# Optimization experiments

Hardware: AMD Instinct MI355X
Metric: run time of the kernel (lower is better)

The kernel has to match this reference:

```python
import jax, jax.numpy as jnp
import numpy as np

# --- fixed model configuration (from init_kwargs) ---
NX, NY, NU, NP = 8, 8, 2, 5
DELTA = 0.01
PHO, CP, AR, AB = 5.0, 6.0, 3.0, 3.0
KR, KB, TD, QR, QB = 2.5, 1.5, 300.0, 200.0, 200.0
CAF, TF = 6.0, 320.0
YMEAN = jnp.array([50.0, 1.0, 0.5, 313.0, 50.0, 1.0, 0.5, 313.0], jnp.float32)
YSTD = jnp.array([2.0, 0.2, 0.1, 4.0, 2.0, 0.2, 0.1, 4.0], jnp.float32)
UMEAN = jnp.array([10.0, 5.0], jnp.float32)
USTD = jnp.array([1.0, 0.5], jnp.float32)


def _fg(x, u):
    """Grey-box CSTR+flash ODE RHS. x: [B,8] scaled, u: [B,2] scaled."""
    x = x * YSTD + YMEAN
    u = u * USTD + UMEAN
    Hr, CAr, CBr, Tr = x[..., 0:1], x[..., 1:2], x[..., 2:3], x[..., 3:4]
    Hb, CAb, CBb, Tb = x[..., 4:5], x[..., 5:6], x[..., 6:7], x[..., 7:8]
    F, D = u[..., 0:1], u[..., 1:2]
    Fr = KR * jnp.sqrt(Hr)
    Fb = KB * jnp.sqrt(Hb)
    dHr = (F + D - Fr) / AR
    dCAr = (F * (CAF - CAr) - D * CAr) / (AR * Hr)
    dCBr = (-F * CBr - D * CBr) / (AR * Hr)
    dTr = (F * (TF - Tr) + D * (TD - Tr)) / (AR * Hr) + QR / (PHO * AR * CP * Hr)
    dHb = (Fr - Fb - D) / AB
    dCAb = (Fr * (CAr - CAb) + D * CAb) / (AB * Hb)
    dCBb = (Fr * (CBr - CBb) + D * CBb) / (AB * Hb)
    dTb = Fr * (Tr - Tb) / (AB * Hb) + QB / (PHO * AB * CP * Hb)
    xdot = jnp.concatenate([dHr, dCAr, dCBr, dTr, dHb, dCAb, dCBb, dTb], axis=-1)
    return xdot / YSTD


def setup_inputs() -> dict:
    key = jax.random.key(0)
    ks = jax.random.split(key, 6)
    B, T = 2048, 128
    d_in, d_h = NX + NP * (NY + NU) + NU, 128  # 60, 128
    useq = jax.random.normal(ks[0], (B, T, NU), jnp.float32)
    xGz0 = jax.random.normal(ks[1], (B, NX + NP * (NY + NU)), jnp.float32)
    W1 = jax.random.normal(ks[2], (d_in, d_h), jnp.float32) * (1.0 / np.sqrt(d_in))
    b1 = jnp.zeros((d_h,), jnp.float32)
    W2 = jax.random.normal(ks[3], (d_h, d_h), jnp.float32) * (1.0 / np.sqrt(d_h))
    b2 = jnp.zeros((d_h,), jnp.float32)
    W3 = jax.random.normal(ks[4], (d_h, NX), jnp.float32) * (1.0 / np.sqrt(d_h))
    b3 = jnp.zeros((NX,), jnp.float32)
    return {"useq": useq, "xGz0": xGz0, "W1": W1, "b1": b1,
            "W2": W2, "b2": b2, "W3": W3, "b3": b3}


def reference(useq, xGz0, W1, b1, W2, b2, W3, b3):
    def fnn(inp):
        h = jnp.tanh(inp @ W1 + b1)
        h = jnp.tanh(h @ W2 + b2)
        return h @ W3 + b3

    def interp(yfull):  # [B,(Np+1)*Ny] -> [B,Np*Ny]
        B = yfull.shape[0]
        y = yfull.reshape(B, NP + 1, NY)
        return (0.5 * (y[:, :-1] + y[:, 1:])).reshape(B, NP * NY)

    def step(xGz, u):
        xG = xGz[:, :NX]
        z = xGz[:, NX:]
        ypseq = z[:, :NP * NY]
        upseq = z[:, NP * NY:]
        # k1
        k1 = _fg(xG, u) + fnn(jnp.concatenate((xG, z, u), axis=-1))
        # interpolated half-step past sequence
        yp_interp = interp(jnp.concatenate((ypseq, xG), axis=-1))
        z_half = jnp.concatenate((yp_interp, upseq), axis=-1)
        x2 = xG + DELTA * (k1 / 2)
        k2 = _fg(x2, u) + fnn(jnp.concatenate((x2, z_half, u), axis=-1))
        x3 = xG + DELTA * (k2 / 2)
        k3 = _fg(x3, u) + fnn(jnp.concatenate((x3, z_half, u), axis=-1))
        yp_shift = jnp.concatenate((ypseq[:, NY:], xG), axis=-1)
        z_full = jnp.concatenate((yp_shift, upseq), axis=-1)
        x4 = xG + DELTA * k3
        k4 = _fg(x4, u) + fnn(jnp.concatenate((x4, z_full, u), axis=-1))
        y = xG
        xGplus = xG + (DELTA / 6) * (k1 + 2 * k2 + 2 * k3 + k4)
        zplus = jnp.concatenate((yp_shift, upseq[:, NU:], u), axis=-1)
        return jnp.concatenate((xGplus, zplus), axis=-1), y

    u_t = jnp.swapaxes(useq, 0, 1)  # [T,B,Nu]
    _, ys = jax.lax.scan(step, xGz0, u_t)  # ys: [T,B,Ny]
    return jnp.swapaxes(ys, 0, 1)  # [B,T,Ny]
```

## Files before the change

### kernel.cpp

```cpp
#include <hip/hip_runtime.h>
#include <math.h>

#define BLOCK 256
#define ROWS 16

typedef __attribute__((ext_vector_type(8))) short s16x8;
typedef __attribute__((ext_vector_type(4))) float f32x4;

static constexpr int O_W1  = 0;
static constexpr int O_W2  = 4608;
static constexpr int O_W3  = 13312;
static constexpr int O_INB = 14400;
static constexpr int O_H1  = 14976;
static constexpr int O_H2  = 16064;
static constexpr int O_B1  = 17152;
static constexpr int O_B2  = 17280;
static constexpr int O_B3  = 17408;
static constexpr int O_SU  = 17416;
static constexpr int O_YPM = 21512;
static constexpr int O_UPM = 22152;
static constexpr int O_XM  = 22344;
static constexpr int O_NNP = 22472;
static constexpr int LDSN  = 22984;

__device__ __forceinline__ unsigned short f2bf(float f) {
  unsigned u = __float_as_uint(f);
  return (unsigned short)((u + 0x7fffu + ((u >> 16) & 1u)) >> 16);
}
__device__ __forceinline__ unsigned cvt_pk_bf16(float lo, float hi) {
  unsigned r;
  asm("v_cvt_pk_bf16_f32 %0, %1, %2" : "=v"(r) : "v"(lo), "v"(hi));
  return r;
}
__device__ __forceinline__ float tanh_fast(float x) {
  float e = __builtin_amdgcn_exp2f(x * 2.88539008177792681f);
  return fmaf(-2.f, __builtin_amdgcn_rcpf(e + 1.f), 1.f);
}

#define MFMA16(A, B, C) __builtin_amdgcn_mfma_f32_16x16x32_bf16((A), (B), (C), 0, 0, 0)

#define PACK_OUT(C, BV, DST) {                        \
  float t0_ = tanh_fast((C)[0] + (BV).x);             \
  float t1_ = tanh_fast((C)[1] + (BV).y);             \
  float t2_ = tanh_fast((C)[2] + (BV).z);             \
  float t3_ = tanh_fast((C)[3] + (BV).w);             \
  uint2 pk_; pk_.x = cvt_pk_bf16(t0_, t1_);           \
  pk_.y = cvt_pk_bf16(t2_, t3_);                      \
  *(uint2*)(DST) = pk_; }

extern "C" __global__ void __launch_bounds__(BLOCK, 1)
cstr_rk4_mfma4(const float* __restrict__ useq, const float* __restrict__ xGz0,
               const float* __restrict__ W1, const float* __restrict__ b1,
               const float* __restrict__ W2, const float* __restrict__ b2,
               const float* __restrict__ W3, const float* __restrict__ b3,
               float* __restrict__ out)
{
  extern __shared__ float smf[];
  unsigned* smu = (unsigned*)smf;
  unsigned short* smh = (unsigned short*)smf;

  unsigned short* w1h = smh + 2 * O_W1;
  unsigned short* w2h = smh + 2 * O_W2;
  unsigned short* w3h = smh + 2 * O_W3;
  unsigned short* inh = smh + 2 * O_INB;
  unsigned short* h1h = smh + 2 * O_H1;
  unsigned short* h2h = smh + 2 * O_H2;
  unsigned* h1u = smu + O_H1;
  unsigned* h2u = smu + O_H2;
  float* b1s = smf + O_B1;
  float* b2s = smf + O_B2;
  float* b3s = smf + O_B3;
  float* su  = smf + O_SU;
  float* ypm = smf + O_YPM;
  float* upm = smf + O_UPM;
  float* xm  = smf + O_XM;
  float* nnp = smf + O_NNP;

  const int tid  = threadIdx.x;
  const int w    = tid >> 6;
  const int l    = tid & 63;
  const int nn   = l & 15;
  const int hh   = l >> 4;
  const int base = blockIdx.x * ROWS;

  for (int i = tid; i < 128 * 72; i += BLOCK) {
    int j = i / 72, k = i % 72;
    w1h[i] = (k < 60) ? f2bf(W1[k * 128 + j]) : (unsigned short)0;
  }
  for (int i = tid; i < 128 * 136; i += BLOCK) {
    int j = i / 136, k = i % 136;
    w2h[i] = (k < 128) ? f2bf(W2[k * 128 + j]) : (unsigned short)0;
  }
  for (int i = tid; i < 16 * 136; i += BLOCK) {
    int o = i / 136, k = i % 136;
    w3h[i] = (o < 8 && k < 128) ? f2bf(W3[k * 8 + o]) : (unsigned short)0;
  }
  if (tid < 128) { b1s[tid] = b1[tid]; b2s[tid] = b2[tid]; }
  if (tid < 8) b3s[tid] = b3[tid];
  for (int i = tid; i < ROWS * 256; i += BLOCK) su[i] = useq[(size_t)base * 256 + i];
  for (int i = tid; i < ROWS * 40; i += BLOCK) {
    int r_ = i / 40, ci = i % 40;
    ypm[i] = xGz0[(size_t)(base + r_) * 58 + 8 + ci];
  }
  for (int i = tid; i < ROWS * 12; i += BLOCK) {
    int r_ = i / 12, ci = i % 12;
    upm[i] = (ci < 10) ? xGz0[(size_t)(base + r_) * 58 + 48 + ci] : 0.f;
  }
  for (int i = tid; i < ROWS * 8; i += BLOCK)
    xm[i] = xGz0[(size_t)(base + (i >> 3)) * 58 + (i & 7)];
  for (int i = tid; i < 16 * 72; i += BLOCK) {
    int n_ = i / 72, k = i % 72;
    unsigned short v = 0;
    if (k < 58)      v = f2bf(xGz0[(size_t)(base + n_) * 58 + k]);
    else if (k < 60) v = f2bf(useq[(size_t)(base + n_) * 256 + (k - 58)]);
    inh[i] = v;
  }

  const int sr = 4 * w + ((l >> 3) & 3);
  const int sc = l & 7;
  const bool st = (l < 32);
  float xg = 0.f, kacc = 0.f, b3r = 0.f;
  if (st) xg = xGz0[(size_t)(base + sr) * 58 + sc];

  __syncthreads();
  if (st) b3r = b3s[sc];

  const int mb0 = 2 * w, mb1 = 2 * w + 1;
  const s16x8 a10 = *(const s16x8*)(w1h + (16 * mb0 + nn) * 72 + 8 * hh);
  const s16x8 a11 = *(const s16x8*)(w1h + (16 * mb0 + nn) * 72 + 32 + 8 * hh);
  const s16x8 a12 = *(const s16x8*)(w1h + (16 * mb1 + nn) * 72 + 8 * hh);
  const s16x8 a13 = *(const s16x8*)(w1h + (16 * mb1 + nn) * 72 + 32 + 8 * hh);
  const s16x8 a200 = *(const s16x8*)(w2h + (16 * mb0 + nn) * 136 +  0 + 8 * hh);
  const s16x8 a201 = *(const s16x8*)(w2h + (16 * mb0 + nn) * 136 + 32 + 8 * hh);
  const s16x8 a202 = *(const s16x8*)(w2h + (16 * mb0 + nn) * 136 + 64 + 8 * hh);
  const s16x8 a203 = *(const s16x8*)(w2h + (16 * mb0 + nn) * 136 + 96 + 8 * hh);
  const s16x8 a210 = *(const s16x8*)(w2h + (16 * mb1 + nn) * 136 +  0 + 8 * hh);
  const s16x8 a211 = *(const s16x8*)(w2h + (16 * mb1 + nn) * 136 + 32 + 8 * hh);
  const s16x8 a212 = *(const s16x8*)(w2h + (16 * mb1 + nn) * 136 + 64 + 8 * hh);
  const s16x8 a213 = *(const s16x8*)(w2h + (16 * mb1 + nn) * 136 + 96 + 8 * hh);
  const s16x8 a3r  = *(const s16x8*)(w3h + nn * 136 + 32 * w + 8 * hh);
  const float4 bva0 = *(const float4*)(b1s + 16 * mb0 + 4 * hh);
  const float4 bva1 = *(const float4*)(b1s + 16 * mb1 + 4 * hh);
  const float4 bvb0 = *(const float4*)(b2s + 16 * mb0 + 4 * hh);
  const float4 bvb1 = *(const float4*)(b2s + 16 * mb1 + 4 * hh);

  const unsigned short* inrow = inh + nn * 72;
  const unsigned short* h1row = h1h + nn * 136;

  #pragma unroll 1
  for (int t = 0; t < 128; ++t) {
    float u0r = 0.f, u1r = 0.f;
    if (st) {
      u0r = su[sr * 256 + 2 * t];
      u1r = su[sr * 256 + 2 * t + 1];
      out[((size_t)(base + sr) * 128 + t) * 8 + sc] = xg;
    }

    #pragma unroll
    for (int s = 0; s < 4; ++s) {
      {
        s16x8 bb0 = *(const s16x8*)(inrow + 8 * hh);
        s16x8 bb1 = *(const s16x8*)(inrow + 32 + 8 * hh);
        f32x4 c1a = (f32x4){0.f, 0.f, 0.f, 0.f};
        f32x4 c1b = (f32x4){0.f, 0.f, 0.f, 0.f};
        c1a = MFMA16(a10, bb0, c1a); c1a = MFMA16(a11, bb1, c1a);
        c1b = MFMA16(a12, bb0, c1b); c1b = MFMA16(a13, bb1, c1b);
        PACK_OUT(c1a, bva0, h1u + nn * 68 + 8 * mb0 + 2 * hh);
        PACK_OUT(c1b, bva1, h1u + nn * 68 + 8 * mb1 + 2 * hh);
      }
      __syncthreads();

      {
        s16x8 q0 = *(const s16x8*)(h1row +  0 + 8 * hh);
        s16x8 q1 = *(const s16x8*)(h1row + 32 + 8 * hh);
        s16x8 q2 = *(const s16x8*)(h1row + 64 + 8 * hh);
        s16x8 q3 = *(const s16x8*)(h1row + 96 + 8 * hh);
        f32x4 c2a = (f32x4){0.f, 0.f, 0.f, 0.f};
        f32x4 c2b = (f32x4){0.f, 0.f, 0.f, 0.f};
        c2a = MFMA16(a200, q0, c2a); c2a = MFMA16(a201, q1, c2a);
        c2a = MFMA16(a202, q2, c2a); c2a = MFMA16(a203, q3, c2a);
        c2b = MFMA16(a210, q0, c2b); c2b = MFMA16(a211, q1, c2b);
        c2b = MFMA16(a212, q2, c2b); c2b = MFMA16(a213, q3, c2b);
        PACK_OUT(c2a, bvb0, h2u + nn * 68 + 8 * mb0 + 2 * hh);
        PACK_OUT(c2b, bvb1, h2u + nn * 68 + 8 * mb1 + 2 * hh);
      }
      __syncthreads();

      {
        s16x8 bf = *(const s16x8*)(h2h + nn * 136 + 32 * w + 8 * hh);
        f32x4 c3 = (f32x4){0.f, 0.f, 0.f, 0.f};
        c3 = MFMA16(a3r, bf, c3);
        if (hh < 2)
          *(float4*)(nnp + w * 128 + nn * 8 + 4 * hh) =
              make_float4(c3[0], c3[1], c3[2], c3[3]);
      }
      __syncthreads();

      if (st) {
        float nv = b3r + nnp[sr * 8 + sc] + nnp[128 + sr * 8 + sc]
                       + nnp[256 + sr * 8 + sc] + nnp[384 + sr * 8 + sc];
        float4 xa = *(const float4*)(xm + sr * 8);
        float4 xb = *(const float4*)(xm + sr * 8 + 4);
        float Hr  = fmaf(xa.x, 2.f, 50.f),  CAr = fmaf(xa.y, 0.2f, 1.f);
        float CBr = fmaf(xa.z, 0.1f, 0.5f), Tr  = fmaf(xa.w, 4.f, 313.f);
        float Hb  = fmaf(xb.x, 2.f, 50.f),  CAb = fmaf(xb.y, 0.2f, 1.f);
        float CBb = fmaf(xb.z, 0.1f, 0.5f), Tb  = fmaf(xb.w, 4.f, 313.f);
        float F = u0r + 10.f, D = fmaf(u1r, 0.5f, 5.f);
        float Fr = 2.5f * sqrtf(Hr), Fb = 1.5f * sqrtf(Hb);
        float rH = __builtin_amdgcn_rcpf(3.f * Hr);
        float rB = __builtin_amdgcn_rcpf(3.f * Hb);
        float k0 = (F + D - Fr) * (1.f / 6.f);
        float k1 = (F * (6.f - CAr) - D * CAr) * (5.f * rH);
        float k2 = (-(F + D) * CBr) * (10.f * rH);
        float k3 = (F * (320.f - Tr) + D * (300.f - Tr)) * (0.25f * rH) + (5.f / 3.f) * rH;
        float k4 = (Fr - Fb - D) * (1.f / 6.f);
        float k5 = (Fr * (CAr - CAb) + D * CAb) * (5.f * rB);
        float k6 = (Fr * (CBr - CBb) + D * CBb) * (10.f * rB);
        float k7 = Fr * (Tr - Tb) * (0.25f * rB) + (5.f / 3.f) * rB;
        float fgc = (sc & 4) ? ((sc & 2) ? ((sc & 1) ? k7 : k6) : ((sc & 1) ? k5 : k4))
                             : ((sc & 2) ? ((sc & 1) ? k3 : k2) : ((sc & 1) ? k1 : k0));
        float kv = fgc + nv;
        float cc;
        if (s == 0)      { kacc = kv;                  cc = fmaf(kv, 0.005f, xg); }
        else if (s == 1) { kacc = fmaf(kv, 2.f, kacc); cc = fmaf(kv, 0.005f, xg); }
        else if (s == 2) { kacc = fmaf(kv, 2.f, kacc); cc = fmaf(kv, 0.01f,  xg); }
        else             { xg = fmaf(kacc + kv, 0.01f / 6.f, xg); cc = xg; }
        inh[sr * 72 + sc] = f2bf(cc);
        xm[sr * 8 + sc] = cc;

        if (s == 0) {
          float a0 = ypm[sr * 40 + sc],      a1 = ypm[sr * 40 + 8 + sc];
          float a2 = ypm[sr * 40 + 16 + sc], a3 = ypm[sr * 40 + 24 + sc];
          float a4 = ypm[sr * 40 + 32 + sc], a5 = xg;
          inh[sr * 72 + 8 + sc]  = f2bf(0.5f * (a0 + a1));
          inh[sr * 72 + 16 + sc] = f2bf(0.5f * (a1 + a2));
          inh[sr * 72 + 24 + sc] = f2bf(0.5f * (a2 + a3));
          inh[sr * 72 + 32 + sc] = f2bf(0.5f * (a3 + a4));
          inh[sr * 72 + 40 + sc] = f2bf(0.5f * (a4 + a5));
        } else if (s == 2) {
          float a1 = ypm[sr * 40 + 8 + sc],  a2 = ypm[sr * 40 + 16 + sc];
          float a3 = ypm[sr * 40 + 24 + sc], a4 = ypm[sr * 40 + 32 + sc];
          float a5 = xg;
          inh[sr * 72 + 8 + sc]  = f2bf(a1);
          inh[sr * 72 + 16 + sc] = f2bf(a2);
          inh[sr * 72 + 24 + sc] = f2bf(a3);
          inh[sr * 72 + 32 + sc] = f2bf(a4);
          inh[sr * 72 + 40 + sc] = f2bf(a5);
          ypm[sr * 40 + sc]      = a1;
          ypm[sr * 40 + 8 + sc]  = a2;
          ypm[sr * 40 + 16 + sc] = a3;
          ypm[sr * 40 + 24 + sc] = a4;
          ypm[sr * 40 + 32 + sc] = a5;
        } else if (s == 3) {
          float nu = upm[sr * 12 + sc + 2];
          upm[sr * 12 + sc] = nu;
          inh[sr * 72 + 48 + sc] = f2bf(nu);
          if (sc < 2) {
            float uv = (sc == 0) ? u0r : u1r;
            upm[sr * 12 + 8 + sc] = uv;
            inh[sr * 72 + 56 + sc] = f2bf(uv);
            if (t < 127)
              inh[sr * 72 + 58 + sc] = f2bf(su[sr * 256 + 2 * (t + 1) + sc]);
          }
        }
      }
      __syncthreads();
    }
  }
}

extern "C" void kernel_launch(void* const* d_in, const int* in_sizes, int n_in,
                              void* d_out, int out_size, void* d_ws, size_t ws_size,
                              hipStream_t stream) {
  const float* useq = (const float*)d_in[0];
  const float* xGz0 = (const float*)d_in[1];
  const float* W1   = (const float*)d_in[2];
  const float* b1   = (const float*)d_in[3];
  const float* W2   = (const float*)d_in[4];
  const float* b2   = (const float*)d_in[5];
  const float* W3   = (const float*)d_in[6];
  const float* b3   = (const float*)d_in[7];
  float* out = (float*)d_out;

  size_t lds = (size_t)LDSN * sizeof(float);
  (void)hipFuncSetAttribute((const void*)cstr_rk4_mfma4,
                            hipFuncAttributeMaxDynamicSharedMemorySize, (int)lds);
  hipLaunchKernelGGL(cstr_rk4_mfma4, dim3(2048 / ROWS), dim3(BLOCK), lds, stream,
                     useq, xGz0, W1, b1, W2, b2, W3, b3, out);
}
```

Baseline: 593.3 us.

## Process four batch rows per block and compute layer-3 redundantly per wave

Each block now handles 4 batch rows instead of 16, so the grid grows from 128 to 512 blocks and the serial 128-step recurrence is spread over more compute units. Every wave now computes the full 128-wide layer-3 reduction itself and reads its row's outputs through cross-lane shuffles, which removes the LDS partial-sum buffer and one barrier per RK stage. The MFMA tiles remain 16 wide, so 12 of every 16 columns are padding, and weight staging into LDS is repeated across four times as many blocks.

Result: slower. 750.6 us (+26.5%).

```diff
diff --git a/kernel.cpp b/kernel.cpp
--- a/kernel.cpp
+++ b/kernel.cpp
@@ -2,7 +2,7 @@
 #include <math.h>
 
 #define BLOCK 256
-#define ROWS 16
+#define ROWS 4
 
 typedef __attribute__((ext_vector_type(8))) short s16x8;
 typedef __attribute__((ext_vector_type(4))) float f32x4;
@@ -17,11 +17,10 @@
 static constexpr int O_B2  = 17280;
 static constexpr int O_B3  = 17408;
 static constexpr int O_SU  = 17416;
-static constexpr int O_YPM = 21512;
-static constexpr int O_UPM = 22152;
-static constexpr int O_XM  = 22344;
-static constexpr int O_NNP = 22472;
-static constexpr int LDSN  = 22984;
+static constexpr int O_YPM = 18440;
+static constexpr int O_UPM = 18600;
+static constexpr int O_XM  = 18648;
+static constexpr int LDSN  = 18680;
 
 __device__ __forceinline__ unsigned short f2bf(float f) {
   unsigned u = __float_as_uint(f);
@@ -49,7 +48,7 @@
   *(uint2*)(DST) = pk_; }
 
 extern "C" __global__ void __launch_bounds__(BLOCK, 1)
-cstr_rk4_mfma4(const float* __restrict__ useq, const float* __restrict__ xGz0,
+cstr_rk4_mfma5(const float* __restrict__ useq, const float* __restrict__ xGz0,
                const float* __restrict__ W1, const float* __restrict__ b1,
                const float* __restrict__ W2, const float* __restrict__ b2,
                const float* __restrict__ W3, const float* __restrict__ b3,
@@ -74,7 +73,6 @@
   float* ypm = smf + O_YPM;
   float* upm = smf + O_UPM;
   float* xm  = smf + O_XM;
-  float* nnp = smf + O_NNP;
 
   const int tid  = threadIdx.x;
   const int w    = tid >> 6;
@@ -111,14 +109,16 @@
   for (int i = tid; i < 16 * 72; i += BLOCK) {
     int n_ = i / 72, k = i % 72;
     unsigned short v = 0;
-    if (k < 58)      v = f2bf(xGz0[(size_t)(base + n_) * 58 + k]);
-    else if (k < 60) v = f2bf(useq[(size_t)(base + n_) * 256 + (k - 58)]);
+    if (n_ < ROWS) {
+      if (k < 58)      v = f2bf(xGz0[(size_t)(base + n_) * 58 + k]);
+      else if (k < 60) v = f2bf(useq[(size_t)(base + n_) * 256 + (k - 58)]);
+    }
     inh[i] = v;
   }
 
-  const int sr = 4 * w + ((l >> 3) & 3);
+  const int sr = w;
   const int sc = l & 7;
-  const bool st = (l < 32);
+  const bool st = (l < 8);
   float xg = 0.f, kacc = 0.f, b3r = 0.f;
   if (st) xg = xGz0[(size_t)(base + sr) * 58 + sc];
 
@@ -138,7 +138,10 @@
   const s16x8 a211 = *(const s16x8*)(w2h + (16 * mb1 + nn) * 136 + 32 + 8 * hh);
   const s16x8 a212 = *(const s16x8*)(w2h + (16 * mb1 + nn) * 136 + 64 + 8 * hh);
   const s16x8 a213 = *(const s16x8*)(w2h + (16 * mb1 + nn) * 136 + 96 + 8 * hh);
-  const s16x8 a3r  = *(const s16x8*)(w3h + nn * 136 + 32 * w + 8 * hh);
+  const s16x8 a30 = *(const s16x8*)(w3h + nn * 136 +  0 + 8 * hh);
+  const s16x8 a31 = *(const s16x8*)(w3h + nn * 136 + 32 + 8 * hh);
+  const s16x8 a32 = *(const s16x8*)(w3h + nn * 136 + 64 + 8 * hh);
+  const s16x8 a33 = *(const s16x8*)(w3h + nn * 136 + 96 + 8 * hh);
   const float4 bva0 = *(const float4*)(b1s + 16 * mb0 + 4 * hh);
   const float4 bva1 = *(const float4*)(b1s + 16 * mb1 + 4 * hh);
   const float4 bvb0 = *(const float4*)(b2s + 16 * mb0 + 4 * hh);
@@ -146,6 +149,9 @@
 
   const unsigned short* inrow = inh + nn * 72;
   const unsigned short* h1row = h1h + nn * 136;
+  const unsigned short* h2row = h2h + nn * 136;
+
+  const int srcl = (((l >> 2) & 1) << 4) + w;
 
   #pragma unroll 1
   for (int t = 0; t < 128; ++t) {
@@ -186,19 +192,23 @@
       }
       __syncthreads();
 
+      f32x4 c3 = (f32x4){0.f, 0.f, 0.f, 0.f};
       {
-        s16x8 bf = *(const s16x8*)(h2h + nn * 136 + 32 * w + 8 * hh);
-        f32x4 c3 = (f32x4){0.f, 0.f, 0.f, 0.f};
-        c3 = MFMA16(a3r, bf, c3);
-        if (hh < 2)
-          *(float4*)(nnp + w * 128 + nn * 8 + 4 * hh) =
-              make_float4(c3[0], c3[1], c3[2], c3[3]);
+        s16x8 p0 = *(const s16x8*)(h2row +  0 + 8 * hh);
+        s16x8 p1 = *(const s16x8*)(h2row + 32 + 8 * hh);
+        s16x8 p2 = *(const s16x8*)(h2row + 64 + 8 * hh);
+        s16x8 p3 = *(const s16x8*)(h2row + 96 + 8 * hh);
+        c3 = MFMA16(a30, p0, c3); c3 = MFMA16(a31, p1, c3);
+        c3 = MFMA16(a32, p2, c3); c3 = MFMA16(a33, p3, c3);
       }
-      __syncthreads();
+      float v0 = __shfl(c3[0], srcl);
+      float v1 = __shfl(c3[1], srcl);
+      float v2 = __shfl(c3[2], srcl);
+      float v3 = __shfl(c3[3], srcl);
 
       if (st) {
-        float nv = b3r + nnp[sr * 8 + sc] + nnp[128 + sr * 8 + sc]
-                       + nnp[256 + sr * 8 + sc] + nnp[384 + sr * 8 + sc];
+        float nv = b3r + ((sc & 2) ? ((sc & 1) ? v3 : v2)
+                                   : ((sc & 1) ? v1 : v0));
         float4 xa = *(const float4*)(xm + sr * 8);
         float4 xb = *(const float4*)(xm + sr * 8 + 4);
         float Hr  = fmaf(xa.x, 2.f, 50.f),  CAr = fmaf(xa.y, 0.2f, 1.f);
@@ -283,8 +293,8 @@
   float* out = (float*)d_out;
 
   size_t lds = (size_t)LDSN * sizeof(float);
-  (void)hipFuncSetAttribute((const void*)cstr_rk4_mfma4,
+  (void)hipFuncSetAttribute((const void*)cstr_rk4_mfma5,
                             hipFuncAttributeMaxDynamicSharedMemorySize, (int)lds);
-  hipLaunchKernelGGL(cstr_rk4_mfma4, dim3(2048 / ROWS), dim3(BLOCK), lds, stream,
+  hipLaunchKernelGGL(cstr_rk4_mfma5, dim3(2048 / ROWS), dim3(BLOCK), lds, stream,
                      useq, xGz0, W1, b1, W2, b2, W3, b3, out);
 }
```
